# Kernel optimization log

Measured on AMD Instinct MI355X. Metric: run time of the kernel, lower is better.

The kernel has to match this reference:

```python
import jax, jax.numpy as jnp
import numpy as np

N = 100000   # nodes
E = 1600000  # edges
IN = 32      # in_channels
H = 64       # hidden_channels
L = 16       # latent_dim
G = 64       # graphs in batch


def setup_inputs() -> dict:
    key = jax.random.key(0)
    ks = jax.random.split(key, 20)
    def w(k, shape, fan):
        return jax.random.normal(k, shape, jnp.float32) * (1.0 / np.sqrt(fan))
    inp = {}
    inp["x"] = jax.random.normal(ks[0], (N, IN), jnp.float32)
    inp["edge_index"] = jax.random.randint(ks[1], (2, E), 0, N)
    inp["batch"] = jnp.sort(jax.random.randint(ks[2], (N,), 0, G))
    # encoder GCN convs: in->h, h->h, h->h
    inp["W_enc0"] = w(ks[3], (IN, H), IN); inp["b_enc0"] = jnp.zeros((H,), jnp.float32)
    inp["W_enc1"] = w(ks[4], (H, H), H);   inp["b_enc1"] = jnp.zeros((H,), jnp.float32)
    inp["W_enc2"] = w(ks[5], (H, H), H);   inp["b_enc2"] = jnp.zeros((H,), jnp.float32)
    # latent projection and decoder projection
    inp["W_proj"] = w(ks[6], (H, L), H);   inp["b_proj"] = jnp.zeros((L,), jnp.float32)
    inp["W_dec_proj"] = w(ks[7], (L, H), L); inp["b_dec_proj"] = jnp.zeros((H,), jnp.float32)
    # decoder GCN convs: h->h, h->in
    inp["W_dec0"] = w(ks[8], (H, H), H);   inp["b_dec0"] = jnp.zeros((H,), jnp.float32)
    inp["W_dec1"] = w(ks[9], (H, IN), H);  inp["b_dec1"] = jnp.zeros((IN,), jnp.float32)
    return inp


def gcn_conv(x, W, b, src, dst, dinv):
    xw = x @ W                                   # [N, out]
    coef = (dinv[src] * dinv[dst])[:, None]      # [E, 1]
    out = jax.ops.segment_sum(xw[src] * coef, dst, num_segments=N)
    out = out + xw * (dinv * dinv)[:, None]      # self-loop contribution
    return out + b


def reference(x, edge_index, batch,
              W_enc0, b_enc0, W_enc1, b_enc1, W_enc2, b_enc2,
              W_proj, b_proj, W_dec_proj, b_dec_proj,
              W_dec0, b_dec0, W_dec1, b_dec1):
    src, dst = edge_index[0], edge_index[1]
    # degree with self-loops (computed on target nodes, PyG default)
    deg = jax.ops.segment_sum(jnp.ones((E,), jnp.float32), dst, num_segments=N) + 1.0
    dinv = jax.lax.rsqrt(deg)
    # encoder (eval mode: dropout is identity)
    h = jax.nn.relu(gcn_conv(x, W_enc0, b_enc0, src, dst, dinv))
    h = jax.nn.relu(gcn_conv(h, W_enc1, b_enc1, src, dst, dinv))
    h = jax.nn.relu(gcn_conv(h, W_enc2, b_enc2, src, dst, dinv))
    # global mean pool over graph ids
    sums = jax.ops.segment_sum(h, batch, num_segments=G)
    cnt = jax.ops.segment_sum(jnp.ones((N,), jnp.float32), batch, num_segments=G)
    g = sums / jnp.maximum(cnt, 1.0)[:, None]    # [G, H]
    z = g @ W_proj + b_proj                      # [G, L]
    # decoder: broadcast z back to nodes, project, two GCN convs
    d = jax.nn.relu(z[batch] @ W_dec_proj + b_dec_proj)
    d = jax.nn.relu(gcn_conv(d, W_dec0, b_dec0, src, dst, dinv))
    x_recon = gcn_conv(d, W_dec1, b_dec1, src, dst, dinv)
    return (x_recon, z)
```

## Files before the change

### kernel.cpp

```cpp
#include <hip/hip_runtime.h>
#include <hip/hip_bf16.h>

typedef unsigned long long u64;

static constexpr int IN_CH  = 32;
static constexpr int HID    = 64;
static constexpr int LAT    = 16;
static constexpr int NGRAPH = 64;
static constexpr int NBUCKET = 1024;
static constexpr int KB_CSR  = 24;


__device__ inline void add4(float4& a, const float4& b) {
    a.x += b.x; a.y += b.y; a.z += b.z; a.w += b.w;
}


__global__ __launch_bounds__(256) void bhist_kernel(const int* __restrict__ ei,
                                                    int* __restrict__ bh, int E) {
    __shared__ int lh[256];
    lh[threadIdx.x] = 0;
    __syncthreads();
    int base = blockIdx.x * 2048;
    #pragma unroll
    for (int j = 0; j < 8; j++) {
        int idx = base + j * 256 + threadIdx.x;
        if (idx < E) atomicAdd(&lh[ei[E + idx] >> 9], 1);
    }
    __syncthreads();
    if (lh[threadIdx.x]) atomicAdd(&bh[threadIdx.x], lh[threadIdx.x]);
}


template <int MODE>
__global__ __launch_bounds__(256) void bin_kernel(
        const int* __restrict__ ei, const u64* __restrict__ sin,
        const int* __restrict__ rank,
        const int* __restrict__ bhv,
        int* __restrict__ gcur,
        u64* __restrict__ sout, int E) {
    __shared__ int lhist[256], lscan[256], lcur[256], gbase[256], bbaseL[256];
    __shared__ u64 sbuf[2048];
    int tid = threadIdx.x;
    lhist[tid] = 0;
    if constexpr (MODE == 0) {
        int v = bhv[tid];
        lscan[tid] = v;
        for (int off = 1; off < 256; off <<= 1) {
            __syncthreads();
            int x = (tid >= off) ? lscan[tid - off] : 0;
            __syncthreads();
            lscan[tid] += x;
        }
        __syncthreads();
        bbaseL[tid] = lscan[tid] - v;
    } else {
        bbaseL[tid] = bhv[tid];
    }
    __syncthreads();
    int base = blockIdx.x * 2048;
    int cnt = min(2048, E - base);
    int myb[8]; u64 myp[8];
    #pragma unroll
    for (int j = 0; j < 8; j++) {
        int idx = base + j * 256 + tid;
        myb[j] = -1;
        if (idx < E) {
            int key, val;
            if constexpr (MODE == 0) { key = ei[E + idx]; val = ei[idx]; }
            else {
                u64 p = sin[idx];
                key = rank[(int)(p >> 32)];
                val = rank[(int)(p & 0xffffffffu)];
            }
            int b = key >> 9;
            myb[j] = b;
            myp[j] = ((u64)(unsigned)key << 32) | (unsigned)val;
            atomicAdd(&lhist[b], 1);
        }
    }
    __syncthreads();
    int v = lhist[tid];
    lscan[tid] = v;
    for (int off = 1; off < 256; off <<= 1) {
        __syncthreads();
        int x = (tid >= off) ? lscan[tid - off] : 0;
        __syncthreads();
        lscan[tid] += x;
    }
    __syncthreads();
    int excl = lscan[tid] - v;
    __syncthreads();
    lscan[tid] = excl;
    lcur[tid] = excl;
    __syncthreads();
    #pragma unroll
    for (int j = 0; j < 8; j++) {
        if (myb[j] >= 0) {
            int pos = atomicAdd(&lcur[myb[j]], 1);
            sbuf[pos] = myp[j];
        }
    }
    gbase[tid] = v ? atomicAdd(&gcur[tid], v) : 0;
    __syncthreads();
    for (int i = tid; i < cnt; i += 256) {
        u64 p = sbuf[i];
        int b = (int)(p >> 41);
        sout[bbaseL[b] + gbase[b] + (i - lscan[b])] = p;
    }
}


__global__ __launch_bounds__(256) void degb_kernel(
        const u64* __restrict__ staged, const int* __restrict__ bh,
        int* __restrict__ cnt, int* __restrict__ hist, int N) {
    __shared__ int ldeg[512];
    __shared__ int lhist[NBUCKET];
    __shared__ int sc[256];
    int b = blockIdx.x;
    int tid = threadIdx.x;
    int bv = bh[tid];
    sc[tid] = bv;
    for (int off = 1; off < 256; off <<= 1) {
        __syncthreads();
        int x = (tid >= off) ? sc[tid - off] : 0;
        __syncthreads();
        sc[tid] += x;
    }
    __syncthreads();
    __shared__ int s0s, s1s;
    if (tid == b) { s0s = sc[b] - bv; s1s = sc[b]; }
    ldeg[tid] = 0;
    ldeg[tid + 256] = 0;
    for (int i = tid; i < NBUCKET; i += 256) lhist[i] = 0;
    __syncthreads();
    int s0 = s0s, s1 = s1s;
    for (int i = s0 + tid; i < s1; i += 256)
        atomicAdd(&ldeg[(int)(staged[i] >> 32) - (b << 9)], 1);
    __syncthreads();
    #pragma unroll
    for (int j = 0; j < 2; j++) {
        int t = tid + j * 256;
        int n = (b << 9) + t;
        if (n < N) {
            int d = ldeg[t];
            cnt[n] = d;
            atomicAdd(&lhist[min(d, NBUCKET - 1)], 1);
        }
    }
    __syncthreads();
    for (int i = tid; i < NBUCKET; i += 256)
        if (lhist[i]) atomicAdd(&hist[i], lhist[i]);
}


__global__ __launch_bounds__(256) void scatter_kernel(
        const int* __restrict__ cnt, const int* __restrict__ batch,
        const int* __restrict__ hist, int* __restrict__ hcur,
        int* __restrict__ perm, int* __restrict__ rank, int* __restrict__ cnt2,
        float* __restrict__ dinvR, float2* __restrict__ pgR, int N) {
    __shared__ int lh[NBUCKET];
    __shared__ int gb[NBUCKET];
    __shared__ int hoff[NBUCKET];
    __shared__ int sc[256];
    int tid = threadIdx.x;
    int h0 = hist[4 * tid], h1 = hist[4 * tid + 1], h2 = hist[4 * tid + 2], h3 = hist[4 * tid + 3];
    int T = h0 + h1 + h2 + h3;
    sc[tid] = T;
    for (int off = 1; off < 256; off <<= 1) {
        __syncthreads();
        int x = (tid >= off) ? sc[tid - off] : 0;
        __syncthreads();
        sc[tid] += x;
    }
    __syncthreads();
    int ex = sc[tid] - T;
    hoff[4 * tid] = ex;
    hoff[4 * tid + 1] = ex + h0;
    hoff[4 * tid + 2] = ex + h0 + h1;
    hoff[4 * tid + 3] = ex + h0 + h1 + h2;
    for (int i = tid; i < NBUCKET; i += 256) lh[i] = 0;
    __syncthreads();
    int n = blockIdx.x * 256 + tid;
    int b = -1, lpos = 0, d = 0;
    if (n < N) {
        d = cnt[n];
        b = min(d, NBUCKET - 1);
        lpos = atomicAdd(&lh[b], 1);
    }
    __syncthreads();
    for (int i = tid; i < NBUCKET; i += 256)
        gb[i] = lh[i] ? atomicAdd(&hcur[i], lh[i]) : 0;
    __syncthreads();
    if (n < N) {
        int r = hoff[b] + gb[b] + lpos;
        perm[r] = n;
        rank[n] = r;
        cnt2[r] = d;
        float dv = rsqrtf((float)d + 1.0f);
        dinvR[r] = dv;
        pgR[r] = make_float2(dv, __int_as_float(batch[n]));
    }
}


__global__ void scan1_kernel(const int* __restrict__ cnt, int* __restrict__ rowptr,
                             int* __restrict__ bsum, int N) {
    __shared__ int s[256];
    int i = blockIdx.x * 256 + threadIdx.x;
    int v = (i < N) ? cnt[i] : 0;
    s[threadIdx.x] = v;
    for (int off = 1; off < 256; off <<= 1) {
        __syncthreads();
        int t = (threadIdx.x >= off) ? s[threadIdx.x - off] : 0;
        __syncthreads();
        s[threadIdx.x] += t;
    }
    if (i < N) rowptr[i] = s[threadIdx.x] - v;
    if (threadIdx.x == 255) bsum[blockIdx.x] = s[255];
}

__global__ __launch_bounds__(256) void scan3_kernel(
        int* __restrict__ rowptr, const int* __restrict__ bsum,
        int* __restrict__ bbaseR, int nb, int N, int E) {
    __shared__ int sc[256];
    int tid = threadIdx.x;
    int v0 = (2 * tid < nb) ? bsum[2 * tid] : 0;
    int v1 = (2 * tid + 1 < nb) ? bsum[2 * tid + 1] : 0;
    int T = v0 + v1;
    sc[tid] = T;
    for (int off = 1; off < 256; off <<= 1) {
        __syncthreads();
        int x = (tid >= off) ? sc[tid - off] : 0;
        __syncthreads();
        sc[tid] += x;
    }
    __syncthreads();
    __shared__ int myoff;
    int blk = blockIdx.x;
    if (tid == (blk >> 1)) {
        int ex = sc[tid] - T;
        myoff = (blk & 1) ? (ex + v0) : ex;
    }
    __syncthreads();
    int i = blk * 256 + tid;
    if (i < N) {
        int v = rowptr[i] + myoff;
        rowptr[i] = v;
        if ((i & 511) == 0) bbaseR[i >> 9] = v;
    }
    if (blk == 0 && tid == 0) {
        for (int t = (N + 511) >> 9; t <= 256; ++t) bbaseR[t] = E;
    }
}


__global__ __launch_bounds__(256) void csr_kernel(
        const u64* __restrict__ staged, const int* __restrict__ bbase,
        const int* __restrict__ rowptr2, int* __restrict__ cur,
        int* __restrict__ col) {
    int bucket = blockIdx.x & 255;
    int k = blockIdx.x >> 8;
    int s0 = bbase[bucket], s1 = bbase[bucket + 1];
    for (int i = s0 + k * 256 + threadIdx.x; i < s1; i += 256 * KB_CSR) {
        u64 p = staged[i];
        int r = (int)(p >> 32);
        int pos = rowptr2[r] + atomicAdd(&cur[r], 1);
        col[pos] = (int)(p & 0xffffffffu);
    }
}


__global__ void slice_x_kernel(const float* __restrict__ x, const int* __restrict__ perm,
                               const float* __restrict__ dinvR,
                               float* __restrict__ xs, int N) {
    int idx = blockIdx.x * 256 + threadIdx.x;
    if (idx >= N * 2) return;
    int r = idx >> 1, h = idx & 1;
    int sl = blockIdx.y;
    int n = perm[r];
    float4 v = ((const float4*)x)[(size_t)n * 8 + sl * 2 + h];
    float dn = dinvR[r];
    v.x *= dn; v.y *= dn; v.z *= dn; v.w *= dn;
    ((float4*)(xs + (size_t)sl * N * 8))[idx] = v;
}


template <int C, bool ADD_BIAS, bool OUT_ROWMAJOR>
__global__ __launch_bounds__(256) void agg_kernel(
        const float* __restrict__ in, float* __restrict__ out,
        const int* __restrict__ rowptr2, const int* __restrict__ cnt2,
        const int* __restrict__ col, const float* __restrict__ dinvR,
        const int* __restrict__ perm, const float* __restrict__ bias, int N) {
    constexpr int NSL = C / 8;
    int sl = blockIdx.x % NSL;
    int nchunks = gridDim.x / NSL;
    int chunk = nchunks - 1 - (blockIdx.x / NSL);
    int slot = threadIdx.x >> 1, h = threadIdx.x & 1;
    int r = chunk * 128 + slot;
    if (r >= N) return;
    const float4* inS = (const float4*)(in + (size_t)sl * N * 8);
    int start = rowptr2[r], m = cnt2[r];
    const int* cp = col + start;
    float4 acc = inS[(size_t)r * 2 + h];
    int i = 0;
    for (; i + 8 <= m; i += 8) {
        int4 cv = *(const int4*)(cp + i + 4 * h);
        int4 ov;
        ov.x = __shfl_xor(cv.x, 1);
        ov.y = __shfl_xor(cv.y, 1);
        ov.z = __shfl_xor(cv.z, 1);
        ov.w = __shfl_xor(cv.w, 1);
        int4 lo = h ? ov : cv;
        int4 hi = h ? cv : ov;
        float4 v0 = inS[(size_t)lo.x * 2 + h], v1 = inS[(size_t)lo.y * 2 + h];
        float4 v2 = inS[(size_t)lo.z * 2 + h], v3 = inS[(size_t)lo.w * 2 + h];
        float4 v4 = inS[(size_t)hi.x * 2 + h], v5 = inS[(size_t)hi.y * 2 + h];
        float4 v6 = inS[(size_t)hi.z * 2 + h], v7 = inS[(size_t)hi.w * 2 + h];
        add4(v0, v1); add4(v2, v3); add4(v4, v5); add4(v6, v7);
        add4(v0, v2); add4(v4, v6);
        add4(acc, v0); add4(acc, v4);
    }
    for (; i < m; ++i) {
        int c = cp[i];
        add4(acc, inS[(size_t)c * 2 + h]);
    }
    float dn = dinvR[r];
    acc.x *= dn; acc.y *= dn; acc.z *= dn; acc.w *= dn;
    if (ADD_BIAS) {
        float4 b4 = ((const float4*)bias)[sl * 2 + h];
        add4(acc, b4);
    }
    if (OUT_ROWMAJOR) ((float4*)out)[(size_t)perm[r] * (C / 4) + sl * 2 + h] = acc;
    else ((float4*)(out + (size_t)sl * N * 8))[(size_t)r * 2 + h] = acc;
}


__global__ __launch_bounds__(256) void gagg_kernel(
        const float* __restrict__ dg, const float2* __restrict__ pgR,
        const int* __restrict__ rowptr2, const int* __restrict__ cnt2,
        const int* __restrict__ col, float* __restrict__ out, int N) {
    __shared__ float dgL[NGRAPH * 68];
    for (int i = threadIdx.x; i < NGRAPH * 64; i += 256)
        dgL[(i >> 6) * 68 + (i & 63)] = dg[i];
    __syncthreads();
    int slot = threadIdx.x >> 1, e = threadIdx.x & 1;
    int r = (gridDim.x - 1 - blockIdx.x) * 128 + slot;
    if (r >= N) return;
    const float4* dgL4 = (const float4*)dgL;
    int start = rowptr2[r], m = cnt2[r];
    const int* cp = col + start;
    float2 ps = pgR[r];
    float dn = ps.x;
    int gs = __float_as_int(ps.y);
    float4 acc[8];
    {
        const float4* rp = dgL4 + gs * 17 + e * 8;
        #pragma unroll
        for (int j = 0; j < 8; ++j) {
            float4 v = rp[j];
            acc[j] = make_float4(dn * v.x, dn * v.y, dn * v.z, dn * v.w);
        }
    }
    int i = 0;
    for (; i + 2 <= m; i += 2) {
        int c0 = cp[i], c1 = cp[i + 1];
        float2 p0 = pgR[c0], p1 = pgR[c1];
        const float4* r0 = dgL4 + __float_as_int(p0.y) * 17 + e * 8;
        const float4* r1 = dgL4 + __float_as_int(p1.y) * 17 + e * 8;
        float w0 = p0.x, w1 = p1.x;
        #pragma unroll
        for (int j = 0; j < 8; ++j) {
            float4 v0 = r0[j], v1 = r1[j];
            acc[j].x += w0 * v0.x + w1 * v1.x;
            acc[j].y += w0 * v0.y + w1 * v1.y;
            acc[j].z += w0 * v0.z + w1 * v1.z;
            acc[j].w += w0 * v0.w + w1 * v1.w;
        }
    }
    if (i < m) {
        int c0 = cp[i];
        float2 p0 = pgR[c0];
        const float4* r0 = dgL4 + __float_as_int(p0.y) * 17 + e * 8;
        float w0 = p0.x;
        #pragma unroll
        for (int j = 0; j < 8; ++j) {
            float4 v0 = r0[j];
            acc[j].x += w0 * v0.x; acc[j].y += w0 * v0.y;
            acc[j].z += w0 * v0.z; acc[j].w += w0 * v0.w;
        }
    }
    #pragma unroll
    for (int k = 0; k < 4; ++k) {
        #pragma unroll
        for (int jj = 0; jj < 2; ++jj) {
            float4 v = acc[k * 2 + jj];
            v.x *= dn; v.y *= dn; v.z *= dn; v.w *= dn;
            ((float4*)(out + (size_t)(4 * e + k) * N * 8))[(size_t)r * 2 + jj] = v;
        }
    }
}


template <int CIN, int COUT, bool RELU, bool BIAS, bool SCALE, bool OUT_ROWMAJOR>
__global__ __launch_bounds__(256) void gemm_kernel(
        const float* __restrict__ in, const float* __restrict__ W,
        const float* __restrict__ b, const float* __restrict__ dinvR,
        const int* __restrict__ perm, float* __restrict__ out, int N) {
    constexpr int NPB = 256 / COUT;
    constexpr int K4 = CIN / 4;
    __shared__ float4 xsh[NPB * K4];
    int r  = threadIdx.x / COUT;
    int co = threadIdx.x % COUT;
    float w[CIN];
    #pragma unroll
    for (int k = 0; k < CIN; ++k) w[k] = W[k * COUT + co];
    float bsv = BIAS ? b[co] : 0.f;
    int ngroups = (N + NPB - 1) / NPB;
    for (int grp = blockIdx.x; grp < ngroups; grp += gridDim.x) {
        int base = grp * NPB;
        __syncthreads();
        for (int i = threadIdx.x; i < NPB * K4; i += 256) {
            int rr = i / K4, k4 = i % K4;
            int n = base + rr;
            float4 v = make_float4(0.f, 0.f, 0.f, 0.f);
            if (n < N) v = ((const float4*)(in + (size_t)(k4 >> 1) * N * 8))[(size_t)n * 2 + (k4 & 1)];
            xsh[i] = v;
        }
        __syncthreads();
        int n = base + r;
        if (n < N) {
            float acc = bsv;
            #pragma unroll
            for (int k4 = 0; k4 < K4; ++k4) {
                float4 xv = xsh[r * K4 + k4];
                acc += xv.x * w[4 * k4] + xv.y * w[4 * k4 + 1]
                     + xv.z * w[4 * k4 + 2] + xv.w * w[4 * k4 + 3];
            }
            if (RELU) acc = fmaxf(acc, 0.f);
            if (SCALE) acc *= dinvR[n];
            if (OUT_ROWMAJOR) out[(size_t)perm[n] * COUT + co] = acc;
            else out[(size_t)(co >> 3) * N * 8 + (size_t)n * 8 + (co & 7)] = acc;
        }
    }
}


__global__ __launch_bounds__(256) void pool_kernel(
        const float* __restrict__ h, const int* __restrict__ batch,
        float* __restrict__ sums, int* __restrict__ cntb, int N) {
    const int CHUNK = 512;
    int chunkStart = blockIdx.x * CHUNK;
    int c = threadIdx.x & 63;
    int r = threadIdx.x >> 6;
    int curg = -1;
    float acc = 0.f;
    int cnt = 0;
    int end = chunkStart + CHUNK;
    if (end > N) end = N;
    for (int n = chunkStart + r; n < end; n += 4) {
        int g = batch[n];
        if (g != curg) {
            if (curg >= 0) {
                atomicAdd(&sums[curg * 64 + c], acc);
                if (c == 0) atomicAdd(&cntb[curg], cnt);
            }
            curg = g; acc = 0.f; cnt = 0;
        }
        acc += h[(size_t)n * 64 + c];
        cnt++;
    }
    if (curg >= 0) {
        atomicAdd(&sums[curg * 64 + c], acc);
        if (c == 0) atomicAdd(&cntb[curg], cnt);
    }
}


__global__ __launch_bounds__(1024) void latent_kernel(
        const float* __restrict__ sums, const int* __restrict__ cntb,
        const float* __restrict__ Wp, const float* __restrict__ bp,
        const float* __restrict__ Wd, const float* __restrict__ bd,
        float* __restrict__ z_out, float* __restrict__ dg) {
    __shared__ float zl[NGRAPH * LAT];
    int t = threadIdx.x;
    {
        int g = t / LAT, l = t % LAT;
        float cf = (float)cntb[g];
        float inv = 1.0f / fmaxf(cf, 1.0f);
        float acc = bp[l];
        #pragma unroll
        for (int k = 0; k < HID; k++) acc += sums[g * HID + k] * inv * Wp[k * LAT + l];
        zl[t] = acc;
        z_out[t] = acc;
    }
    __syncthreads();
    #pragma unroll
    for (int i = 0; i < 4; i++) {
        int idx = t + i * 1024;
        int g = idx >> 6, c = idx & 63;
        float acc = bd[c];
        #pragma unroll
        for (int l = 0; l < LAT; l++) acc += zl[g * LAT + l] * Wd[l * HID + c];
        dg[idx] = fmaxf(acc, 0.f);
    }
}


extern "C" void kernel_launch(void* const* d_in, const int* in_sizes, int n_in,
                              void* d_out, int out_size, void* d_ws, size_t ws_size,
                              hipStream_t stream) {
    const float* x          = (const float*)d_in[0];
    const int*   ei         = (const int*)d_in[1];
    const int*   batch      = (const int*)d_in[2];
    const float* W_enc0     = (const float*)d_in[3];
    const float* b_enc0     = (const float*)d_in[4];
    const float* W_enc1     = (const float*)d_in[5];
    const float* b_enc1     = (const float*)d_in[6];
    const float* W_enc2     = (const float*)d_in[7];
    const float* b_enc2     = (const float*)d_in[8];
    const float* W_proj     = (const float*)d_in[9];
    const float* b_proj     = (const float*)d_in[10];
    const float* W_dec_proj = (const float*)d_in[11];
    const float* b_dec_proj = (const float*)d_in[12];
    const float* W_dec0     = (const float*)d_in[13];
    const float* b_dec0     = (const float*)d_in[14];
    const float* W_dec1     = (const float*)d_in[15];
    const float* b_dec1     = (const float*)d_in[16];

    const int N = in_sizes[0] / IN_CH;
    const int E = in_sizes[1] / 2;

    char* ws = (char*)d_ws;
    size_t off = 0;
    auto alloc = [&](size_t bytes) {
        void* p = ws + off;
        off += (bytes + 255) & ~(size_t)255;
        return p;
    };
    float* A       = (float*)alloc((size_t)N * HID * 4);
    float* B       = (float*)alloc((size_t)N * HID * 4);
    float* XS      = (float*)alloc((size_t)N * IN_CH * 4);
    int*   col     = (int*)  alloc((size_t)E * 4);
    int*   cntn    = (int*)  alloc((size_t)N * 4);
    int*   cnt2    = (int*)  alloc((size_t)N * 4);
    int*   rowptr2 = (int*)  alloc((size_t)(N + 1) * 4);
    int*   perm    = (int*)  alloc((size_t)N * 4);
    int*   rank    = (int*)  alloc((size_t)N * 4);
    float* dinvR   = (float*)alloc((size_t)N * 4);
    float2* pgR    = (float2*)alloc((size_t)N * 8);
    int nb = (N + 255) / 256;
    int*   bsum    = (int*)  alloc((size_t)nb * 4);
    int*   bbaseR  = (int*)  alloc(257 * 4);
    char* zbase = ws + off;
    int*   cursor  = (int*)  alloc((size_t)N * 4);
    int*   hist    = (int*)  alloc((size_t)NBUCKET * 4);
    int*   hcur    = (int*)  alloc((size_t)NBUCKET * 4);
    int*   bh      = (int*)  alloc(256 * 4);
    int*   gcurD   = (int*)  alloc(256 * 4);
    int*   gcurR   = (int*)  alloc(256 * 4);
    float* sums    = (float*)alloc((size_t)NGRAPH * HID * 4);
    int*   cntb    = (int*)  alloc((size_t)NGRAPH * 4);
    size_t zbytes = (size_t)((ws + off) - zbase);
    float* dg      = (float*)alloc((size_t)NGRAPH * HID * 4);

    u64* staged1 = (u64*)XS;
    u64* staged2 = (u64*)A;

    float* x_recon = (float*)d_out;
    float* z_out   = (float*)d_out + (size_t)N * IN_CH;

    hipMemsetAsync(zbase, 0, zbytes, stream);

    int ebins = (E + 2047) / 2048;
    int chunks = (N + 127) / 128;

    bhist_kernel<<<ebins, 256, 0, stream>>>(ei, bh, E);
    bin_kernel<0><<<ebins, 256, 0, stream>>>(ei, nullptr, nullptr, bh, gcurD, staged1, E);
    degb_kernel<<<256, 256, 0, stream>>>(staged1, bh, cntn, hist, N);
    scatter_kernel<<<nb, 256, 0, stream>>>(cntn, batch, hist, hcur, perm, rank, cnt2,
                                           dinvR, pgR, N);
    scan1_kernel<<<nb, 256, 0, stream>>>(cnt2, rowptr2, bsum, N);
    scan3_kernel<<<nb, 256, 0, stream>>>(rowptr2, bsum, bbaseR, nb, N, E);
    bin_kernel<1><<<ebins, 256, 0, stream>>>(nullptr, staged1, rank, bbaseR, gcurR, staged2, E);
    csr_kernel<<<256 * KB_CSR, 256, 0, stream>>>(staged2, bbaseR, rowptr2, cursor, col);

    {
        dim3 g((N * 2 + 255) / 256, IN_CH / 8);
        slice_x_kernel<<<g, 256, 0, stream>>>(x, perm, dinvR, XS, N);
    }

    agg_kernel<IN_CH, false, false><<<chunks * 4, 256, 0, stream>>>(
        XS, A, rowptr2, cnt2, col, dinvR, perm, nullptr, N);
    gemm_kernel<IN_CH, HID, true, true, true, false><<<2048, 256, 0, stream>>>(
        A, W_enc0, b_enc0, dinvR, perm, B, N);
    agg_kernel<HID, false, false><<<chunks * 8, 256, 0, stream>>>(
        B, A, rowptr2, cnt2, col, dinvR, perm, nullptr, N);
    gemm_kernel<HID, HID, true, true, true, false><<<2048, 256, 0, stream>>>(
        A, W_enc1, b_enc1, dinvR, perm, B, N);
    agg_kernel<HID, false, false><<<chunks * 8, 256, 0, stream>>>(
        B, A, rowptr2, cnt2, col, dinvR, perm, nullptr, N);
    gemm_kernel<HID, HID, true, true, false, true><<<2048, 256, 0, stream>>>(
        A, W_enc2, b_enc2, dinvR, perm, B, N);

    pool_kernel<<<(N + 511) / 512, 256, 0, stream>>>(B, batch, sums, cntb, N);
    latent_kernel<<<1, 1024, 0, stream>>>(sums, cntb, W_proj, b_proj, W_dec_proj, b_dec_proj, z_out, dg);

    gagg_kernel<<<chunks, 256, 0, stream>>>(dg, pgR, rowptr2, cnt2, col, A, N);
    gemm_kernel<HID, HID, true, true, false, false><<<2048, 256, 0, stream>>>(
        A, W_dec0, b_dec0, dinvR, perm, B, N);
    gemm_kernel<HID, IN_CH, false, false, true, false><<<2048, 256, 0, stream>>>(
        B, W_dec1, nullptr, dinvR, perm, A, N);
    agg_kernel<IN_CH, true, true><<<chunks * 4, 256, 0, stream>>>(
        A, x_recon, rowptr2, cnt2, col, dinvR, perm, b_dec1, N);
}
```

Baseline: 699.0 us.

## Sort nodes by degree within 512-node buckets instead of globally

Replaces the global degree-sort pipeline (degree histogram, global scatter, two-pass scan, second edge binning) with a per-bucket local degree sort inside degb_kernel, which also computes rowptr, rank, perm and dinv directly. The CSR build now reads the first staged edge array and maps endpoints through rank, removing a whole edge re-binning pass and four kernel launches. It also drops the reversed chunk order and the shuffle-based column loading in the aggregation kernels, and adds a 4-wide tail step there. Load balance in aggregation is now only local within each bucket rather than global, which may change wave behaviour.

```diff
diff --git a/kernel.cpp b/kernel.cpp
--- a/kernel.cpp
+++ b/kernel.cpp
@@ -7,7 +7,6 @@
 static constexpr int HID    = 64;
 static constexpr int LAT    = 16;
 static constexpr int NGRAPH = 64;
-static constexpr int NBUCKET = 1024;
 static constexpr int KB_CSR  = 24;
 
 
@@ -32,19 +31,15 @@
 }
 
 
-template <int MODE>
 __global__ __launch_bounds__(256) void bin_kernel(
-        const int* __restrict__ ei, const u64* __restrict__ sin,
-        const int* __restrict__ rank,
-        const int* __restrict__ bhv,
-        int* __restrict__ gcur,
-        u64* __restrict__ sout, int E) {
+        const int* __restrict__ ei, const int* __restrict__ bh,
+        int* __restrict__ gcur, u64* __restrict__ sout, int E) {
     __shared__ int lhist[256], lscan[256], lcur[256], gbase[256], bbaseL[256];
     __shared__ u64 sbuf[2048];
     int tid = threadIdx.x;
     lhist[tid] = 0;
-    if constexpr (MODE == 0) {
-        int v = bhv[tid];
+    {
+        int v = bh[tid];
         lscan[tid] = v;
         for (int off = 1; off < 256; off <<= 1) {
             __syncthreads();
@@ -54,8 +49,6 @@
         }
         __syncthreads();
         bbaseL[tid] = lscan[tid] - v;
-    } else {
-        bbaseL[tid] = bhv[tid];
     }
     __syncthreads();
     int base = blockIdx.x * 2048;
@@ -66,13 +59,7 @@
         int idx = base + j * 256 + tid;
         myb[j] = -1;
         if (idx < E) {
-            int key, val;
-            if constexpr (MODE == 0) { key = ei[E + idx]; val = ei[idx]; }
-            else {
-                u64 p = sin[idx];
-                key = rank[(int)(p >> 32)];
-                val = rank[(int)(p & 0xffffffffu)];
-            }
+            int key = ei[E + idx], val = ei[idx];
             int b = key >> 9;
             myb[j] = b;
             myp[j] = ((u64)(unsigned)key << 32) | (unsigned)val;
@@ -113,160 +100,121 @@
 
 __global__ __launch_bounds__(256) void degb_kernel(
         const u64* __restrict__ staged, const int* __restrict__ bh,
-        int* __restrict__ cnt, int* __restrict__ hist, int N) {
-    __shared__ int ldeg[512];
-    __shared__ int lhist[NBUCKET];
+        const int* __restrict__ batch,
+        int* __restrict__ rank, int* __restrict__ perm, int* __restrict__ cnt2,
+        int* __restrict__ rowptr2, float* __restrict__ dinvR,
+        float2* __restrict__ pgR, int* __restrict__ bbase, int N, int E) {
     __shared__ int sc[256];
-    int b = blockIdx.x;
-    int tid = threadIdx.x;
-    int bv = bh[tid];
-    sc[tid] = bv;
-    for (int off = 1; off < 256; off <<= 1) {
-        __syncthreads();
-        int x = (tid >= off) ? sc[tid - off] : 0;
-        __syncthreads();
-        sc[tid] += x;
-    }
-    __syncthreads();
+    __shared__ int ldeg[512], lrank[512], degS[512], psum[512];
+    __shared__ int kcur[256];
     __shared__ int s0s, s1s;
-    if (tid == b) { s0s = sc[b] - bv; s1s = sc[b]; }
-    ldeg[tid] = 0;
-    ldeg[tid + 256] = 0;
-    for (int i = tid; i < NBUCKET; i += 256) lhist[i] = 0;
+    int b = blockIdx.x, tid = threadIdx.x;
+    {
+        int bv = bh[tid];
+        sc[tid] = bv;
+        for (int off = 1; off < 256; off <<= 1) {
+            __syncthreads();
+            int x = (tid >= off) ? sc[tid - off] : 0;
+            __syncthreads();
+            sc[tid] += x;
+        }
+        __syncthreads();
+        if (tid == b) { s0s = sc[tid] - bv; s1s = sc[tid]; }
+    }
+    ldeg[tid] = 0; ldeg[tid + 256] = 0;
+    degS[tid] = 0; degS[tid + 256] = 0;
+    kcur[tid] = 0;
     __syncthreads();
     int s0 = s0s, s1 = s1s;
+    int base = b << 9;
     for (int i = s0 + tid; i < s1; i += 256)
-        atomicAdd(&ldeg[(int)(staged[i] >> 32) - (b << 9)], 1);
-    __syncthreads();
+        atomicAdd(&ldeg[(int)(__builtin_nontemporal_load(&staged[i]) >> 32) - base], 1);
+    __syncthreads();
+    int k = N - base; k = k < 0 ? 0 : (k > 512 ? 512 : k);
     #pragma unroll
     for (int j = 0; j < 2; j++) {
         int t = tid + j * 256;
-        int n = (b << 9) + t;
-        if (n < N) {
-            int d = ldeg[t];
-            cnt[n] = d;
-            atomicAdd(&lhist[min(d, NBUCKET - 1)], 1);
-        }
-    }
-    __syncthreads();
-    for (int i = tid; i < NBUCKET; i += 256)
-        if (lhist[i]) atomicAdd(&hist[i], lhist[i]);
-}
-
-
-__global__ __launch_bounds__(256) void scatter_kernel(
-        const int* __restrict__ cnt, const int* __restrict__ batch,
-        const int* __restrict__ hist, int* __restrict__ hcur,
-        int* __restrict__ perm, int* __restrict__ rank, int* __restrict__ cnt2,
-        float* __restrict__ dinvR, float2* __restrict__ pgR, int N) {
-    __shared__ int lh[NBUCKET];
-    __shared__ int gb[NBUCKET];
-    __shared__ int hoff[NBUCKET];
-    __shared__ int sc[256];
-    int tid = threadIdx.x;
-    int h0 = hist[4 * tid], h1 = hist[4 * tid + 1], h2 = hist[4 * tid + 2], h3 = hist[4 * tid + 3];
-    int T = h0 + h1 + h2 + h3;
-    sc[tid] = T;
-    for (int off = 1; off < 256; off <<= 1) {
-        __syncthreads();
-        int x = (tid >= off) ? sc[tid - off] : 0;
-        __syncthreads();
-        sc[tid] += x;
-    }
-    __syncthreads();
-    int ex = sc[tid] - T;
-    hoff[4 * tid] = ex;
-    hoff[4 * tid + 1] = ex + h0;
-    hoff[4 * tid + 2] = ex + h0 + h1;
-    hoff[4 * tid + 3] = ex + h0 + h1 + h2;
-    for (int i = tid; i < NBUCKET; i += 256) lh[i] = 0;
-    __syncthreads();
-    int n = blockIdx.x * 256 + tid;
-    int b = -1, lpos = 0, d = 0;
-    if (n < N) {
-        d = cnt[n];
-        b = min(d, NBUCKET - 1);
-        lpos = atomicAdd(&lh[b], 1);
-    }
-    __syncthreads();
-    for (int i = tid; i < NBUCKET; i += 256)
-        gb[i] = lh[i] ? atomicAdd(&hcur[i], lh[i]) : 0;
-    __syncthreads();
-    if (n < N) {
-        int r = hoff[b] + gb[b] + lpos;
-        perm[r] = n;
-        rank[n] = r;
-        cnt2[r] = d;
-        float dv = rsqrtf((float)d + 1.0f);
-        dinvR[r] = dv;
-        pgR[r] = make_float2(dv, __int_as_float(batch[n]));
-    }
-}
-
-
-__global__ void scan1_kernel(const int* __restrict__ cnt, int* __restrict__ rowptr,
-                             int* __restrict__ bsum, int N) {
-    __shared__ int s[256];
-    int i = blockIdx.x * 256 + threadIdx.x;
-    int v = (i < N) ? cnt[i] : 0;
-    s[threadIdx.x] = v;
-    for (int off = 1; off < 256; off <<= 1) {
-        __syncthreads();
-        int t = (threadIdx.x >= off) ? s[threadIdx.x - off] : 0;
-        __syncthreads();
-        s[threadIdx.x] += t;
-    }
-    if (i < N) rowptr[i] = s[threadIdx.x] - v;
-    if (threadIdx.x == 255) bsum[blockIdx.x] = s[255];
-}
-
-__global__ __launch_bounds__(256) void scan3_kernel(
-        int* __restrict__ rowptr, const int* __restrict__ bsum,
-        int* __restrict__ bbaseR, int nb, int N, int E) {
-    __shared__ int sc[256];
-    int tid = threadIdx.x;
-    int v0 = (2 * tid < nb) ? bsum[2 * tid] : 0;
-    int v1 = (2 * tid + 1 < nb) ? bsum[2 * tid + 1] : 0;
-    int T = v0 + v1;
-    sc[tid] = T;
-    for (int off = 1; off < 256; off <<= 1) {
-        __syncthreads();
-        int x = (tid >= off) ? sc[tid - off] : 0;
-        __syncthreads();
-        sc[tid] += x;
-    }
-    __syncthreads();
-    __shared__ int myoff;
-    int blk = blockIdx.x;
-    if (tid == (blk >> 1)) {
+        if (t < k) atomicAdd(&kcur[min(ldeg[t], 255)], 1);
+    }
+    __syncthreads();
+    {
+        int hv = kcur[tid];
+        sc[tid] = hv;
+        for (int off = 1; off < 256; off <<= 1) {
+            __syncthreads();
+            int x = (tid >= off) ? sc[tid - off] : 0;
+            __syncthreads();
+            sc[tid] += x;
+        }
+        __syncthreads();
+        kcur[tid] = sc[tid] - hv;
+    }
+    __syncthreads();
+    #pragma unroll
+    for (int j = 0; j < 2; j++) {
+        int t = tid + j * 256;
+        if (t < k) lrank[t] = atomicAdd(&kcur[min(ldeg[t], 255)], 1);
+    }
+    __syncthreads();
+    #pragma unroll
+    for (int j = 0; j < 2; j++) {
+        int t = tid + j * 256;
+        if (t < k) degS[lrank[t]] = ldeg[t];
+    }
+    __syncthreads();
+    {
+        int v0 = degS[2 * tid], v1 = degS[2 * tid + 1];
+        int T = v0 + v1;
+        sc[tid] = T;
+        for (int off = 1; off < 256; off <<= 1) {
+            __syncthreads();
+            int x = (tid >= off) ? sc[tid - off] : 0;
+            __syncthreads();
+            sc[tid] += x;
+        }
+        __syncthreads();
         int ex = sc[tid] - T;
-        myoff = (blk & 1) ? (ex + v0) : ex;
-    }
-    __syncthreads();
-    int i = blk * 256 + tid;
-    if (i < N) {
-        int v = rowptr[i] + myoff;
-        rowptr[i] = v;
-        if ((i & 511) == 0) bbaseR[i >> 9] = v;
-    }
-    if (blk == 0 && tid == 0) {
-        for (int t = (N + 511) >> 9; t <= 256; ++t) bbaseR[t] = E;
+        psum[2 * tid] = ex;
+        psum[2 * tid + 1] = ex + v0;
+    }
+    __syncthreads();
+    #pragma unroll
+    for (int j = 0; j < 2; j++) {
+        int t = tid + j * 256;
+        if (t < k) {
+            int n = base + t;
+            int d = ldeg[t], lr = lrank[t];
+            int r = base + lr;
+            rank[n] = r;
+            perm[r] = n;
+            cnt2[r] = d;
+            rowptr2[r] = s0 + psum[lr];
+            float dv = rsqrtf((float)d + 1.0f);
+            dinvR[r] = dv;
+            pgR[r] = make_float2(dv, __int_as_float(batch[n]));
+        }
+    }
+    if (tid == 0) {
+        bbase[b] = s0;
+        if (b == 255) bbase[256] = E;
     }
 }
 
 
 __global__ __launch_bounds__(256) void csr_kernel(
         const u64* __restrict__ staged, const int* __restrict__ bbase,
-        const int* __restrict__ rowptr2, int* __restrict__ cur,
-        int* __restrict__ col) {
+        const int* __restrict__ rank, const int* __restrict__ rowptr2,
+        int* __restrict__ cur, int* __restrict__ col) {
     int bucket = blockIdx.x & 255;
     int k = blockIdx.x >> 8;
     int s0 = bbase[bucket], s1 = bbase[bucket + 1];
     for (int i = s0 + k * 256 + threadIdx.x; i < s1; i += 256 * KB_CSR) {
-        u64 p = staged[i];
-        int r = (int)(p >> 32);
-        int pos = rowptr2[r] + atomicAdd(&cur[r], 1);
-        col[pos] = (int)(p & 0xffffffffu);
+        u64 p = __builtin_nontemporal_load(&staged[i]);
+        int dst = (int)(p >> 32);
+        int src = (int)(p & 0xffffffffu);
+        int rd = rank[dst];
+        int pos = rowptr2[rd] + atomicAdd(&cur[rd], 1);
+        col[pos] = rank[src];
     }
 }
 
@@ -294,8 +242,7 @@
         const int* __restrict__ perm, const float* __restrict__ bias, int N) {
     constexpr int NSL = C / 8;
     int sl = blockIdx.x % NSL;
-    int nchunks = gridDim.x / NSL;
-    int chunk = nchunks - 1 - (blockIdx.x / NSL);
+    int chunk = blockIdx.x / NSL;
     int slot = threadIdx.x >> 1, h = threadIdx.x & 1;
     int r = chunk * 128 + slot;
     if (r >= N) return;
@@ -305,21 +252,23 @@
     float4 acc = inS[(size_t)r * 2 + h];
     int i = 0;
     for (; i + 8 <= m; i += 8) {
-        int4 cv = *(const int4*)(cp + i + 4 * h);
-        int4 ov;
-        ov.x = __shfl_xor(cv.x, 1);
-        ov.y = __shfl_xor(cv.y, 1);
-        ov.z = __shfl_xor(cv.z, 1);
-        ov.w = __shfl_xor(cv.w, 1);
-        int4 lo = h ? ov : cv;
-        int4 hi = h ? cv : ov;
-        float4 v0 = inS[(size_t)lo.x * 2 + h], v1 = inS[(size_t)lo.y * 2 + h];
-        float4 v2 = inS[(size_t)lo.z * 2 + h], v3 = inS[(size_t)lo.w * 2 + h];
-        float4 v4 = inS[(size_t)hi.x * 2 + h], v5 = inS[(size_t)hi.y * 2 + h];
-        float4 v6 = inS[(size_t)hi.z * 2 + h], v7 = inS[(size_t)hi.w * 2 + h];
+        int s0 = cp[i], s1 = cp[i+1], s2 = cp[i+2], s3 = cp[i+3];
+        int s4 = cp[i+4], s5 = cp[i+5], s6 = cp[i+6], s7 = cp[i+7];
+        float4 v0 = inS[(size_t)s0*2+h], v1 = inS[(size_t)s1*2+h];
+        float4 v2 = inS[(size_t)s2*2+h], v3 = inS[(size_t)s3*2+h];
+        float4 v4 = inS[(size_t)s4*2+h], v5 = inS[(size_t)s5*2+h];
+        float4 v6 = inS[(size_t)s6*2+h], v7 = inS[(size_t)s7*2+h];
         add4(v0, v1); add4(v2, v3); add4(v4, v5); add4(v6, v7);
         add4(v0, v2); add4(v4, v6);
         add4(acc, v0); add4(acc, v4);
+    }
+    if (i + 4 <= m) {
+        int s0 = cp[i], s1 = cp[i+1], s2 = cp[i+2], s3 = cp[i+3];
+        float4 v0 = inS[(size_t)s0*2+h], v1 = inS[(size_t)s1*2+h];
+        float4 v2 = inS[(size_t)s2*2+h], v3 = inS[(size_t)s3*2+h];
+        add4(v0, v1); add4(v2, v3); add4(v0, v2);
+        add4(acc, v0);
+        i += 4;
     }
     for (; i < m; ++i) {
         int c = cp[i];
@@ -345,7 +294,7 @@
         dgL[(i >> 6) * 68 + (i & 63)] = dg[i];
     __syncthreads();
     int slot = threadIdx.x >> 1, e = threadIdx.x & 1;
-    int r = (gridDim.x - 1 - blockIdx.x) * 128 + slot;
+    int r = blockIdx.x * 128 + slot;
     if (r >= N) return;
     const float4* dgL4 = (const float4*)dgL;
     int start = rowptr2[r], m = cnt2[r];
@@ -542,30 +491,23 @@
     float* B       = (float*)alloc((size_t)N * HID * 4);
     float* XS      = (float*)alloc((size_t)N * IN_CH * 4);
     int*   col     = (int*)  alloc((size_t)E * 4);
-    int*   cntn    = (int*)  alloc((size_t)N * 4);
     int*   cnt2    = (int*)  alloc((size_t)N * 4);
     int*   rowptr2 = (int*)  alloc((size_t)(N + 1) * 4);
     int*   perm    = (int*)  alloc((size_t)N * 4);
     int*   rank    = (int*)  alloc((size_t)N * 4);
     float* dinvR   = (float*)alloc((size_t)N * 4);
     float2* pgR    = (float2*)alloc((size_t)N * 8);
-    int nb = (N + 255) / 256;
-    int*   bsum    = (int*)  alloc((size_t)nb * 4);
-    int*   bbaseR  = (int*)  alloc(257 * 4);
+    int*   bbase   = (int*)  alloc(257 * 4);
     char* zbase = ws + off;
     int*   cursor  = (int*)  alloc((size_t)N * 4);
-    int*   hist    = (int*)  alloc((size_t)NBUCKET * 4);
-    int*   hcur    = (int*)  alloc((size_t)NBUCKET * 4);
     int*   bh      = (int*)  alloc(256 * 4);
     int*   gcurD   = (int*)  alloc(256 * 4);
-    int*   gcurR   = (int*)  alloc(256 * 4);
     float* sums    = (float*)alloc((size_t)NGRAPH * HID * 4);
     int*   cntb    = (int*)  alloc((size_t)NGRAPH * 4);
     size_t zbytes = (size_t)((ws + off) - zbase);
     float* dg      = (float*)alloc((size_t)NGRAPH * HID * 4);
 
     u64* staged1 = (u64*)XS;
-    u64* staged2 = (u64*)A;
 
     float* x_recon = (float*)d_out;
     float* z_out   = (float*)d_out + (size_t)N * IN_CH;
@@ -576,14 +518,10 @@
     int chunks = (N + 127) / 128;
 
     bhist_kernel<<<ebins, 256, 0, stream>>>(ei, bh, E);
-    bin_kernel<0><<<ebins, 256, 0, stream>>>(ei, nullptr, nullptr, bh, gcurD, staged1, E);
-    degb_kernel<<<256, 256, 0, stream>>>(staged1, bh, cntn, hist, N);
-    scatter_kernel<<<nb, 256, 0, stream>>>(cntn, batch, hist, hcur, perm, rank, cnt2,
-                                           dinvR, pgR, N);
-    scan1_kernel<<<nb, 256, 0, stream>>>(cnt2, rowptr2, bsum, N);
-    scan3_kernel<<<nb, 256, 0, stream>>>(rowptr2, bsum, bbaseR, nb, N, E);
-    bin_kernel<1><<<ebins, 256, 0, stream>>>(nullptr, staged1, rank, bbaseR, gcurR, staged2, E);
-    csr_kernel<<<256 * KB_CSR, 256, 0, stream>>>(staged2, bbaseR, rowptr2, cursor, col);
+    bin_kernel<<<ebins, 256, 0, stream>>>(ei, bh, gcurD, staged1, E);
+    degb_kernel<<<256, 256, 0, stream>>>(staged1, bh, batch, rank, perm, cnt2,
+                                         rowptr2, dinvR, pgR, bbase, N, E);
+    csr_kernel<<<256 * KB_CSR, 256, 0, stream>>>(staged1, bbase, rank, rowptr2, cursor, col);
 
     {
         dim3 g((N * 2 + 255) / 256, IN_CH / 8);
```

After: 686.2 us. Within noise of the previous version (-1.8%).
